# Optimization experiments

Measured on AMD Instinct MI355X. Metric: run time of the kernel, lower is better.

The kernel has to match this reference:

```python
import jax, jax.numpy as jnp
import numpy as np

ALPHA = 0.2  # leakyrelu negative slope and residual scale


def setup_inputs() -> dict:
    key = jax.random.key(0)
    k1, k2, k3, k4 = jax.random.split(key, 4)
    B, N, C, F = 8, 2048, 128, 128
    text = jax.random.normal(k1, (B, N, C), dtype=jnp.float32)
    adj = jax.random.uniform(k2, (B, N, N), dtype=jnp.float32)  # unused by the layer's math
    W = jax.random.normal(k3, (C, F), dtype=jnp.float32) * (1.0 / np.sqrt(C))
    a = jax.random.normal(k4, (2 * F, 1), dtype=jnp.float32) * 0.1
    return {"text": text, "adj": adj, "W": W, "a": a}


def reference(text, adj, W, a):
    # h: [B, N, F]
    h = jnp.matmul(text, W)
    Fdim = W.shape[1]
    a1 = a[:Fdim, 0]  # applies to source node i
    a2 = a[Fdim:, 0]  # applies to target node j
    e1 = jnp.einsum('bnf,f->bn', h, a1)  # [B, N]
    e2 = jnp.einsum('bnf,f->bn', h, a2)  # [B, N]
    # scores[b,i,j] = leakyrelu(a1.h_i + a2.h_j)  (same as concat-matmul in original)
    scores = jax.nn.leaky_relu(e1[:, :, None] + e2[:, None, :], negative_slope=ALPHA)
    attention = jax.nn.softmax(scores, axis=2)  # [B, N, N]; dropout off (eval)
    h_prime = jnp.matmul(attention, h)  # [B, N, F]
    return jax.nn.elu(h_prime + ALPHA * h)
```

## Files before the change

### kernel.cpp

```cpp
#include <hip/hip_runtime.h>
#include <hip/hip_bf16.h>

#define BB 8
#define NN 2048
#define CC 128
#define FF 128
#define ALPHA 0.2f
#define ROWS 16
#define WTPAD 136
#define CHN 256
#define CLEN 8
#define CSH 3

typedef __hip_bfloat16 bf16;
typedef __attribute__((ext_vector_type(8))) short short8;
typedef __attribute__((ext_vector_type(4))) float f32x4;
typedef unsigned long long u64;

__device__ __forceinline__ float ld1(const void* p, int i, int f32) {
    if (f32) return ((const float*)p)[i];
    return __bfloat162float(((const bf16*)p)[i]);
}
__device__ __forceinline__ float2 ld2(const void* p, int pair, int f32) {
    if (f32) return ((const float2*)p)[pair];
    __hip_bfloat162 v = ((const __hip_bfloat162*)p)[pair];
    return make_float2(__bfloat162float(v.x), __bfloat162float(v.y));
}
__device__ __forceinline__ u64 shfl_xor_u64(u64 v, int mask) {
    int lo = (int)(unsigned)(v & 0xFFFFFFFFull);
    int hi = (int)(unsigned)(v >> 32);
    lo = __shfl_xor(lo, mask, 64);
    hi = __shfl_xor(hi, mask, 64);
    return ((u64)(unsigned)hi << 32) | (unsigned)lo;
}

__global__ __launch_bounds__(256) void k_prep(const void* __restrict__ text,
                                              const void* __restrict__ W,
                                              const void* __restrict__ a,
                                              int* __restrict__ flag,
                                              float* __restrict__ wa1,
                                              float* __restrict__ wa2,
                                              ushort* __restrict__ WT) {
    __shared__ int cnt;
    __shared__ float aL[2 * FF];
    const int t = threadIdx.x;
    if (t == 0) cnt = 0;
    __syncthreads();
    const ushort2* p = (const ushort2*)text;
    int local = 0;
    for (int i = t; i < 1024; i += 256) {
        ushort2 v = p[i];
        float f = __uint_as_float(((unsigned)v.x) << 16);
        if (!(fabsf(f) <= 100.f)) local++;
    }
    atomicAdd(&cnt, local);
    __syncthreads();
    const int f32 = (cnt >= 64) ? 1 : 0;

    if (blockIdx.x == 0) {
        if (t == 0) flag[0] = f32;
        aL[t] = ld1(a, t, f32);
        __syncthreads();
        if (t < CC) {
            float s1 = 0.f, s2 = 0.f;
            for (int f = 0; f < FF; f += 4) {
                float w0 = ld1(W, t * FF + f, f32);
                float w1 = ld1(W, t * FF + f + 1, f32);
                float w2 = ld1(W, t * FF + f + 2, f32);
                float w3 = ld1(W, t * FF + f + 3, f32);
                s1 += w0 * aL[f] + w1 * aL[f + 1] + w2 * aL[f + 2] + w3 * aL[f + 3];
                s2 += w0 * aL[FF + f] + w1 * aL[FF + f + 1] + w2 * aL[FF + f + 2] + w3 * aL[FF + f + 3];
            }
            wa1[t] = s1; wa2[t] = s2;
        }
    } else {
        const int base = (blockIdx.x - 1) * 2048;
        for (int i = 0; i < 8; ++i) {
            int idx = base + i * 256 + t;
            int cc = idx >> 7, f = idx & 127;
            float v = ld1(W, idx, f32);
            bf16 b = __float2bfloat16(v);
            WT[f * CC + cc] = *(const ushort*)&b;
        }
    }
}

__global__ __launch_bounds__(256) void k_e(const void* __restrict__ text,
                                           const float* __restrict__ wa1,
                                           const float* __restrict__ wa2,
                                           float* __restrict__ e1,
                                           float* __restrict__ e2,
                                           const int* __restrict__ flag) {
    const int f32 = *flag;
    const int wave = threadIdx.x >> 6;
    const int lane = threadIdx.x & 63;
    const int row = blockIdx.x * 4 + wave;
    float2 tv = ld2(text, row * (CC / 2) + lane, f32);
    float s1 = tv.x * wa1[2 * lane] + tv.y * wa1[2 * lane + 1];
    float s2 = tv.x * wa2[2 * lane] + tv.y * wa2[2 * lane + 1];
#pragma unroll
    for (int off = 32; off > 0; off >>= 1) {
        s1 += __shfl_down(s1, off, 64);
        s2 += __shfl_down(s2, off, 64);
    }
    if (lane == 0) { e1[row] = s1; e2[row] = s2; }
}

__global__ __launch_bounds__(1024) void k_sort(const float* __restrict__ e2,
                                               const float* __restrict__ e1,
                                               float* __restrict__ e2s,
                                               int* __restrict__ sidx,
                                               float* __restrict__ rig) {
    __shared__ u64 lk[NN];
    __shared__ float es[NN];
    __shared__ float Z1L[NN + 1];
    __shared__ float Z2L[NN + 1];
    __shared__ float2 wtot[16];
    __shared__ float2 woff[16];
    const int b = blockIdx.x;
    const int t = threadIdx.x;

    float f0 = e2[b * NN + 2 * t], f1 = e2[b * NN + 2 * t + 1];
    unsigned m0 = __float_as_uint(f0); m0 = (m0 & 0x80000000u) ? ~m0 : (m0 | 0x80000000u);
    unsigned m1 = __float_as_uint(f1); m1 = (m1 & 0x80000000u) ? ~m1 : (m1 | 0x80000000u);
    u64 s0 = ((u64)m0 << 32) | (unsigned)(2 * t);
    u64 s1 = ((u64)m1 << 32) | (unsigned)(2 * t + 1);

    for (int size = 2; size <= NN; size <<= 1) {
        const bool up = (((2 * t) & size) == 0);
        for (int stride = size >> 1; stride >= 1; stride >>= 1) {
            if (stride == 1) {
                u64 mn = s0 < s1 ? s0 : s1;
                u64 mx = s0 < s1 ? s1 : s0;
                s0 = up ? mn : mx;
                s1 = up ? mx : mn;
            } else if (stride <= 64) {
                const int m = stride >> 1;
                u64 p0 = shfl_xor_u64(s0, m);
                u64 p1 = shfl_xor_u64(s1, m);
                const bool keepmin = (((t & m) == 0) == up);
                s0 = keepmin ? (s0 < p0 ? s0 : p0) : (s0 < p0 ? p0 : s0);
                s1 = keepmin ? (s1 < p1 ? s1 : p1) : (s1 < p1 ? p1 : s1);
            } else {
                lk[2 * t] = s0; lk[2 * t + 1] = s1;
                __syncthreads();
                u64 p0 = lk[(2 * t) ^ stride];
                u64 p1 = lk[(2 * t + 1) ^ stride];
                const bool keepmin = ((((2 * t) & stride) == 0) == up);
                s0 = keepmin ? (s0 < p0 ? s0 : p0) : (s0 < p0 ? p0 : s0);
                s1 = keepmin ? (s1 < p1 ? s1 : p1) : (s1 < p1 ? p1 : s1);
                __syncthreads();
            }
        }
    }

    unsigned k0 = (unsigned)(s0 >> 32), k1 = (unsigned)(s1 >> 32);
    float v0 = __uint_as_float((k0 & 0x80000000u) ? (k0 ^ 0x80000000u) : ~k0);
    float v1 = __uint_as_float((k1 & 0x80000000u) ? (k1 ^ 0x80000000u) : ~k1);
    es[2 * t] = v0;  es[2 * t + 1] = v1;
    e2s[b * NN + 2 * t] = v0;
    e2s[b * NN + 2 * t + 1] = v1;
    sidx[b * NN + 2 * t] = (int)(unsigned)(s0 & 0xFFFFFFFFull);
    sidx[b * NN + 2 * t + 1] = (int)(unsigned)(s1 & 0xFFFFFFFFull);

    float x0a = expf(v0), x0b = expf(ALPHA * v0);
    float x1a = expf(v1), x1b = expf(ALPHA * v1);
    float pa = x0a + x1a, pb = x0b + x1b;
    float sa = pa, sb = pb;
    const int lane = t & 63, wid = t >> 6;
#pragma unroll
    for (int off = 1; off < 64; off <<= 1) {
        float ya = __shfl_up(sa, off, 64);
        float yb = __shfl_up(sb, off, 64);
        if (lane >= off) { sa += ya; sb += yb; }
    }
    if (lane == 63) wtot[wid] = make_float2(sa, sb);
    __syncthreads();
    if (t == 0) {
        float ra = 0.f, rb = 0.f;
        for (int w2 = 0; w2 < 16; ++w2) {
            float2 tt = wtot[w2];
            woff[w2] = make_float2(ra, rb);
            ra += tt.x; rb += tt.y;
        }
    }
    __syncthreads();
    float2 o = woff[wid];
    float pre_a = o.x + sa - pa, pre_b = o.y + sb - pb;
    if (t == 0) { Z1L[0] = 0.f; Z2L[0] = 0.f; }
    Z1L[2 * t + 1] = pre_a + x0a;  Z2L[2 * t + 1] = pre_b + x0b;
    Z1L[2 * t + 2] = pre_a + pa;   Z2L[2 * t + 2] = pre_b + pb;
    __syncthreads();

    const float ZN = Z1L[NN];
#pragma unroll
    for (int rr = 0; rr < 2; ++rr) {
        const int r = t + rr * 1024;
        float ev = e1[b * NN + r];
        float w1 = expf(ev), w2 = expf(ALPHA * ev);
        float thr = -ev;
        int lo = 0, hi = NN;
        while (lo < hi) {
            int mid = (lo + hi) >> 1;
            if (es[mid] <= thr) lo = mid + 1; else hi = mid;
        }
        float den = w1 * (ZN - Z1L[lo]) + w2 * Z2L[lo];
        den = fmaxf(den, 1e-30f);
        ((float4*)rig)[b * NN + r] = make_float4(__int_as_float(lo), w1, w2, 1.f / den);
    }
}

__global__ __launch_bounds__(128) void k_tot(const void* __restrict__ text,
                                             const float* __restrict__ e2s,
                                             const int* __restrict__ sidx,
                                             float* __restrict__ T1,
                                             float* __restrict__ T2,
                                             const int* __restrict__ flag) {
    const int f32 = *flag;
    const int b = blockIdx.x / CHN, ch = blockIdx.x % CHN;
    const int c = threadIdx.x;
    float r1 = 0.f, r2 = 0.f;
    const int k0 = ch * CLEN;
#pragma unroll
    for (int kk = 0; kk < CLEN; ++kk) {
        int k = k0 + kk;
        float v = e2s[b * NN + k];
        int j = sidx[b * NN + k];
        float x = ld1(text, (b * NN + j) * CC + c, f32);
        r1 += expf(v) * x;
        r2 += expf(ALPHA * v) * x;
    }
    T1[(b * (CHN + 1) + ch) * CC + c] = r1;
    T2[(b * (CHN + 1) + ch) * CC + c] = r2;
}

__global__ __launch_bounds__(256) void k_scan2(float* __restrict__ T1,
                                               float* __restrict__ T2) {
    __shared__ float2 wt[4];
    const int b = blockIdx.x >> 7, c = blockIdx.x & 127;
    const int ch = threadIdx.x;
    float* P1 = T1 + (size_t)(b * (CHN + 1)) * CC + c;
    float* P2 = T2 + (size_t)(b * (CHN + 1)) * CC + c;
    const float t1 = P1[ch * CC];
    const float t2 = P2[ch * CC];
    float s1 = t1, s2 = t2;
    const int lane = ch & 63, wid = ch >> 6;
#pragma unroll
    for (int off = 1; off < 64; off <<= 1) {
        float y1 = __shfl_up(s1, off, 64);
        float y2 = __shfl_up(s2, off, 64);
        if (lane >= off) { s1 += y1; s2 += y2; }
    }
    if (lane == 63) wt[wid] = make_float2(s1, s2);
    __syncthreads();
    float o1 = 0.f, o2 = 0.f;
#pragma unroll
    for (int w2 = 0; w2 < 4; ++w2)
        if (w2 < wid) { o1 += wt[w2].x; o2 += wt[w2].y; }
    P1[ch * CC] = o1 + s1 - t1;
    P2[ch * CC] = o2 + s2 - t2;
    if (ch == CHN - 1) { P1[CHN * CC] = o1 + s1; P2[CHN * CC] = o2 + s2; }
}

__global__ __launch_bounds__(256) void k_out(const void* __restrict__ text,
                                             const ushort* __restrict__ WT,
                                             const float* __restrict__ T1,
                                             const float* __restrict__ T2,
                                             const float* __restrict__ e2s,
                                             const int* __restrict__ sidx,
                                             const float* __restrict__ rig,
                                             void* __restrict__ out,
                                             const int* __restrict__ flag) {
    __shared__ ushort WTl[FF * WTPAD];
    __shared__ ushort ul[ROWS * WTPAD];
    __shared__ float4 ri[ROWS];
    const int f32 = *flag;
    const int t = threadIdx.x;
    const int b = blockIdx.x / (NN / ROWS);
    const int r0 = (blockIdx.x % (NN / ROWS)) * ROWS;

    {
        const uint4* src = (const uint4*)WT;
#pragma unroll
        for (int i = 0; i < 8; ++i) {
            int idx = i * 256 + t;
            uint4 v = src[idx];
            int f = idx >> 4, cb = idx & 15;
            *(uint4*)&WTl[f * WTPAD + cb * 8] = v;
        }
    }
    if (t < ROWS) ri[t] = ((const float4*)rig)[b * NN + r0 + t];
    __syncthreads();

    {
        const int c = t & 127;
        const int g = t >> 7;
        const float* CB1 = T1 + (size_t)(b * (CHN + 1)) * CC + c;
        const float* CB2 = T2 + (size_t)(b * (CHN + 1)) * CC + c;
        const float* e2sb = e2s + b * NN;
        const int* sxb = sidx + b * NN;
        const float S1 = CB1[CHN * CC];
#pragma unroll
        for (int q = 0; q < 8; ++q) {
            const int rr = g * 8 + q;
            float4 info = ri[rr];
            const int k = __builtin_amdgcn_readfirstlane(__float_as_int(info.x));
            const int c0 = k >> CSH;
            float P1 = CB1[c0 * CC];
            float P2 = CB2[c0 * CC];
            const int j0 = c0 * CLEN;
            const int cnt = k - j0;
            if (cnt > 0) {
                float vv[CLEN - 1]; int jj[CLEN - 1];
#pragma unroll
                for (int i = 0; i < CLEN - 1; ++i) {
                    vv[i] = e2sb[j0 + i];
                    jj[i] = sxb[j0 + i];
                }
#pragma unroll
                for (int i = 0; i < CLEN - 1; ++i) {
                    if (i < cnt) {
                        float x = ld1(text, (b * NN + jj[i]) * CC + c, f32);
                        P1 += expf(vv[i]) * x;
                        P2 += expf(ALPHA * vv[i]) * x;
                    }
                }
            }
            float tc = ld1(text, (b * NN + r0 + rr) * CC + c, f32);
            float u = (info.y * (S1 - P1) + info.z * P2) * info.w + ALPHA * tc;
            bf16 ub = __float2bfloat16(u);
            ul[rr * WTPAD + c] = *(const ushort*)&ub;
        }
    }
    __syncthreads();

    {
        const int wv = t >> 6;
        const int lane = t & 63;
        const int m = lane & 15;
        const int quad = lane >> 4;
        f32x4 acc0 = {0.f, 0.f, 0.f, 0.f};
        f32x4 acc1 = {0.f, 0.f, 0.f, 0.f};
        const int f0 = (wv * 2 + 0) * 16 + m;
        const int f1 = (wv * 2 + 1) * 16 + m;
#pragma unroll
        for (int kt = 0; kt < 4; ++kt) {
            const int ko = kt * 32 + quad * 8;
            short8 afrag = *(const short8*)&ul[m * WTPAD + ko];
            short8 bf0 = *(const short8*)&WTl[f0 * WTPAD + ko];
            short8 bf1 = *(const short8*)&WTl[f1 * WTPAD + ko];
            acc0 = __builtin_amdgcn_mfma_f32_16x16x32_bf16(afrag, bf0, acc0, 0, 0, 0);
            acc1 = __builtin_amdgcn_mfma_f32_16x16x32_bf16(afrag, bf1, acc1, 0, 0, 0);
        }
#pragma unroll
        for (int ft = 0; ft < 2; ++ft) {
            f32x4 acc = ft ? acc1 : acc0;
            const int f = (wv * 2 + ft) * 16 + m;
#pragma unroll
            for (int reg = 0; reg < 4; ++reg) {
                const int urow = quad * 4 + reg;
                float x = acc[reg];
                float y = x > 0.f ? x : expm1f(x);
                const int orow = b * NN + r0 + urow;
                if (f32) ((float*)out)[orow * FF + f] = y;
                else     ((bf16*)out)[orow * FF + f] = __float2bfloat16(y);
            }
        }
    }
}

extern "C" void kernel_launch(void* const* d_in, const int* in_sizes, int n_in,
                              void* d_out, int out_size, void* d_ws, size_t ws_size,
                              hipStream_t stream) {
    const void* text = d_in[0];
    const void* Wp   = (n_in >= 4) ? d_in[2] : d_in[1];
    const void* ap   = (n_in >= 4) ? d_in[3] : d_in[2];
    for (int i = 0; i < n_in; ++i) {
        int s = in_sizes[i];
        if (s == BB * NN * CC)      text = d_in[i];
        else if (s == CC * FF)      Wp = d_in[i];
        else if (s == 2 * FF)       ap = d_in[i];
    }

    float* w = (float*)d_ws;
    size_t off = 0;
    int*    flagp  = (int*)(w + off);      off += 16;
    float*  wa1    = w + off;              off += 128;
    float*  wa2    = w + off;              off += 128;
    ushort* WT     = (ushort*)(w + off);   off += 8192;
    float*  e1     = w + off;              off += BB * NN;
    float*  e2     = w + off;              off += BB * NN;
    float*  e2s    = w + off;              off += BB * NN;
    int*    sidx   = (int*)(w + off);      off += BB * NN;
    float*  rig    = w + off;              off += (size_t)4 * BB * NN;
    float*  T1     = w + off;              off += (size_t)BB * (CHN + 1) * CC;
    float*  T2     = w + off;              off += (size_t)BB * (CHN + 1) * CC;

    k_prep<<<9, 256, 0, stream>>>(text, Wp, ap, flagp, wa1, wa2, WT);
    k_e<<<BB * NN / 4, 256, 0, stream>>>(text, wa1, wa2, e1, e2, flagp);
    k_sort<<<BB, 1024, 0, stream>>>(e2, e1, e2s, sidx, rig);
    k_tot<<<BB * CHN, 128, 0, stream>>>(text, e2s, sidx, T1, T2, flagp);
    k_scan2<<<BB * CC, 256, 0, stream>>>(T1, T2);
    k_out<<<BB * NN / ROWS, 256, 0, stream>>>(text, WT, T1, T2, e2s, sidx,
                                              rig, d_out, flagp);
}
```

Before: 248.2 us.

## Fuse chunk-total, scan and output kernels into one cooperative persistent kernel

Merges the three trailing kernels (per-chunk totals, prefix scan, output with MFMA projection) into a single cooperative kernel. Grid-wide syncs separate the phases, and grid-stride loops cover the work. It also loads the W tile into LDS once per block instead of once per 16-row tile. This targets kernel launch gaps and repeated WT loads, at the cost of grid.sync overhead and a smaller persistent grid. If the cooperative launch fails, it falls back to three phase-specific launches.

Result: slower. 438.9 us (+76.8%).

```diff
diff --git a/kernel.cpp b/kernel.cpp
--- a/kernel.cpp
+++ b/kernel.cpp
@@ -1,5 +1,8 @@
 #include <hip/hip_runtime.h>
 #include <hip/hip_bf16.h>
+#include <hip/hip_cooperative_groups.h>
+
+namespace cg = cooperative_groups;
 
 #define BB 8
 #define NN 2048
@@ -210,76 +213,25 @@
     }
 }
 
-__global__ __launch_bounds__(128) void k_tot(const void* __restrict__ text,
-                                             const float* __restrict__ e2s,
-                                             const int* __restrict__ sidx,
-                                             float* __restrict__ T1,
-                                             float* __restrict__ T2,
-                                             const int* __restrict__ flag) {
-    const int f32 = *flag;
-    const int b = blockIdx.x / CHN, ch = blockIdx.x % CHN;
-    const int c = threadIdx.x;
-    float r1 = 0.f, r2 = 0.f;
-    const int k0 = ch * CLEN;
-#pragma unroll
-    for (int kk = 0; kk < CLEN; ++kk) {
-        int k = k0 + kk;
-        float v = e2s[b * NN + k];
-        int j = sidx[b * NN + k];
-        float x = ld1(text, (b * NN + j) * CC + c, f32);
-        r1 += expf(v) * x;
-        r2 += expf(ALPHA * v) * x;
-    }
-    T1[(b * (CHN + 1) + ch) * CC + c] = r1;
-    T2[(b * (CHN + 1) + ch) * CC + c] = r2;
-}
-
-__global__ __launch_bounds__(256) void k_scan2(float* __restrict__ T1,
-                                               float* __restrict__ T2) {
-    __shared__ float2 wt[4];
-    const int b = blockIdx.x >> 7, c = blockIdx.x & 127;
-    const int ch = threadIdx.x;
-    float* P1 = T1 + (size_t)(b * (CHN + 1)) * CC + c;
-    float* P2 = T2 + (size_t)(b * (CHN + 1)) * CC + c;
-    const float t1 = P1[ch * CC];
-    const float t2 = P2[ch * CC];
-    float s1 = t1, s2 = t2;
-    const int lane = ch & 63, wid = ch >> 6;
-#pragma unroll
-    for (int off = 1; off < 64; off <<= 1) {
-        float y1 = __shfl_up(s1, off, 64);
-        float y2 = __shfl_up(s2, off, 64);
-        if (lane >= off) { s1 += y1; s2 += y2; }
-    }
-    if (lane == 63) wt[wid] = make_float2(s1, s2);
-    __syncthreads();
-    float o1 = 0.f, o2 = 0.f;
-#pragma unroll
-    for (int w2 = 0; w2 < 4; ++w2)
-        if (w2 < wid) { o1 += wt[w2].x; o2 += wt[w2].y; }
-    P1[ch * CC] = o1 + s1 - t1;
-    P2[ch * CC] = o2 + s2 - t2;
-    if (ch == CHN - 1) { P1[CHN * CC] = o1 + s1; P2[CHN * CC] = o2 + s2; }
-}
-
-__global__ __launch_bounds__(256) void k_out(const void* __restrict__ text,
-                                             const ushort* __restrict__ WT,
-                                             const float* __restrict__ T1,
-                                             const float* __restrict__ T2,
-                                             const float* __restrict__ e2s,
-                                             const int* __restrict__ sidx,
-                                             const float* __restrict__ rig,
-                                             void* __restrict__ out,
-                                             const int* __restrict__ flag) {
+__global__ __launch_bounds__(256, 4) void k_fused(const void* __restrict__ text,
+                                                  const ushort* __restrict__ WT,
+                                                  float* __restrict__ T1,
+                                                  float* __restrict__ T2,
+                                                  const float* __restrict__ e2s,
+                                                  const int* __restrict__ sidx,
+                                                  const float* __restrict__ rig,
+                                                  void* __restrict__ out,
+                                                  const int* __restrict__ flag,
+                                                  int plo, int phi) {
+    cg::grid_group grid = cg::this_grid();
     __shared__ ushort WTl[FF * WTPAD];
     __shared__ ushort ul[ROWS * WTPAD];
     __shared__ float4 ri[ROWS];
+    __shared__ float2 wt[4];
+    const int t = threadIdx.x;
     const int f32 = *flag;
-    const int t = threadIdx.x;
-    const int b = blockIdx.x / (NN / ROWS);
-    const int r0 = (blockIdx.x % (NN / ROWS)) * ROWS;
-
-    {
+
+    if (phi >= 2) {
         const uint4* src = (const uint4*)WT;
 #pragma unroll
         for (int i = 0; i < 8; ++i) {
@@ -289,82 +241,142 @@
             *(uint4*)&WTl[f * WTPAD + cb * 8] = v;
         }
     }
-    if (t < ROWS) ri[t] = ((const float4*)rig)[b * NN + r0 + t];
-    __syncthreads();
-
-    {
-        const int c = t & 127;
-        const int g = t >> 7;
-        const float* CB1 = T1 + (size_t)(b * (CHN + 1)) * CC + c;
-        const float* CB2 = T2 + (size_t)(b * (CHN + 1)) * CC + c;
-        const float* e2sb = e2s + b * NN;
-        const int* sxb = sidx + b * NN;
-        const float S1 = CB1[CHN * CC];
-#pragma unroll
-        for (int q = 0; q < 8; ++q) {
-            const int rr = g * 8 + q;
-            float4 info = ri[rr];
-            const int k = __builtin_amdgcn_readfirstlane(__float_as_int(info.x));
-            const int c0 = k >> CSH;
-            float P1 = CB1[c0 * CC];
-            float P2 = CB2[c0 * CC];
-            const int j0 = c0 * CLEN;
-            const int cnt = k - j0;
-            if (cnt > 0) {
-                float vv[CLEN - 1]; int jj[CLEN - 1];
-#pragma unroll
-                for (int i = 0; i < CLEN - 1; ++i) {
-                    vv[i] = e2sb[j0 + i];
-                    jj[i] = sxb[j0 + i];
+
+    if (plo <= 0 && 0 <= phi) {
+        for (int it = blockIdx.x; it < BB * CHN / 2; it += gridDim.x) {
+            const int gch = it * 2 + (t >> 7);
+            const int b = gch >> 8, ch = gch & (CHN - 1);
+            const int c = t & 127;
+            float r1 = 0.f, r2 = 0.f;
+            const int k0 = ch * CLEN;
+#pragma unroll
+            for (int kk = 0; kk < CLEN; ++kk) {
+                int k = k0 + kk;
+                float v = e2s[b * NN + k];
+                int j = sidx[b * NN + k];
+                float x = ld1(text, (b * NN + j) * CC + c, f32);
+                r1 += expf(v) * x;
+                r2 += expf(ALPHA * v) * x;
+            }
+            T1[(b * (CHN + 1) + ch) * CC + c] = r1;
+            T2[(b * (CHN + 1) + ch) * CC + c] = r2;
+        }
+    }
+    if (plo <= 0 && 1 <= phi) grid.sync();
+
+    if (plo <= 1 && 1 <= phi) {
+        for (int it = blockIdx.x; it < BB * CC; it += gridDim.x) {
+            const int b = it >> 7, c = it & 127;
+            const int ch = t;
+            float* P1 = T1 + (size_t)(b * (CHN + 1)) * CC + c;
+            float* P2 = T2 + (size_t)(b * (CHN + 1)) * CC + c;
+            const float t1 = P1[ch * CC];
+            const float t2 = P2[ch * CC];
+            float s1 = t1, s2 = t2;
+            const int lane = ch & 63, wid = ch >> 6;
+#pragma unroll
+            for (int off = 1; off < 64; off <<= 1) {
+                float y1 = __shfl_up(s1, off, 64);
+                float y2 = __shfl_up(s2, off, 64);
+                if (lane >= off) { s1 += y1; s2 += y2; }
+            }
+            if (lane == 63) wt[wid] = make_float2(s1, s2);
+            __syncthreads();
+            float o1 = 0.f, o2 = 0.f;
+#pragma unroll
+            for (int w2 = 0; w2 < 4; ++w2)
+                if (w2 < wid) { o1 += wt[w2].x; o2 += wt[w2].y; }
+            P1[ch * CC] = o1 + s1 - t1;
+            P2[ch * CC] = o2 + s2 - t2;
+            if (ch == CHN - 1) { P1[CHN * CC] = o1 + s1; P2[CHN * CC] = o2 + s2; }
+            __syncthreads();
+        }
+    }
+    if (plo <= 1 && 2 <= phi) grid.sync();
+
+    if (plo <= 2 && 2 <= phi) {
+        for (int it = blockIdx.x; it < BB * NN / ROWS; it += gridDim.x) {
+            const int b = it / (NN / ROWS);
+            const int r0 = (it % (NN / ROWS)) * ROWS;
+            if (t < ROWS) ri[t] = ((const float4*)rig)[b * NN + r0 + t];
+            __syncthreads();
+
+            {
+                const int c = t & 127;
+                const int g = t >> 7;
+                const float* CB1 = T1 + (size_t)(b * (CHN + 1)) * CC + c;
+                const float* CB2 = T2 + (size_t)(b * (CHN + 1)) * CC + c;
+                const float* e2sb = e2s + b * NN;
+                const int* sxb = sidx + b * NN;
+                const float S1 = CB1[CHN * CC];
+#pragma unroll
+                for (int q = 0; q < 8; ++q) {
+                    const int rr = g * 8 + q;
+                    float4 info = ri[rr];
+                    const int k = __builtin_amdgcn_readfirstlane(__float_as_int(info.x));
+                    const int c0 = k >> CSH;
+                    float P1 = CB1[c0 * CC];
+                    float P2 = CB2[c0 * CC];
+                    const int j0 = c0 * CLEN;
+                    const int cnt = k - j0;
+                    if (cnt > 0) {
+                        float vv[CLEN - 1]; int jj[CLEN - 1];
+#pragma unroll
+                        for (int i = 0; i < CLEN - 1; ++i) {
+                            vv[i] = e2sb[j0 + i];
+                            jj[i] = sxb[j0 + i];
+                        }
+#pragma unroll
+                        for (int i = 0; i < CLEN - 1; ++i) {
+                            if (i < cnt) {
+                                float x = ld1(text, (b * NN + jj[i]) * CC + c, f32);
+                                P1 += expf(vv[i]) * x;
+                                P2 += expf(ALPHA * vv[i]) * x;
+                            }
+                        }
+                    }
+                    float tc = ld1(text, (b * NN + r0 + rr) * CC + c, f32);
+                    float u = (info.y * (S1 - P1) + info.z * P2) * info.w + ALPHA * tc;
+                    bf16 ub = __float2bfloat16(u);
+                    ul[rr * WTPAD + c] = *(const ushort*)&ub;
                 }
-#pragma unroll
-                for (int i = 0; i < CLEN - 1; ++i) {
-                    if (i < cnt) {
-                        float x = ld1(text, (b * NN + jj[i]) * CC + c, f32);
-                        P1 += expf(vv[i]) * x;
-                        P2 += expf(ALPHA * vv[i]) * x;
+            }
+            __syncthreads();
+
+            {
+                const int wv = t >> 6;
+                const int lane = t & 63;
+                const int m = lane & 15;
+                const int quad = lane >> 4;
+                f32x4 acc0 = {0.f, 0.f, 0.f, 0.f};
+                f32x4 acc1 = {0.f, 0.f, 0.f, 0.f};
+                const int f0 = (wv * 2 + 0) * 16 + m;
+                const int f1 = (wv * 2 + 1) * 16 + m;
+#pragma unroll
+                for (int kt = 0; kt < 4; ++kt) {
+                    const int ko = kt * 32 + quad * 8;
+                    short8 afrag = *(const short8*)&ul[m * WTPAD + ko];
+                    short8 bf0 = *(const short8*)&WTl[f0 * WTPAD + ko];
+                    short8 bf1 = *(const short8*)&WTl[f1 * WTPAD + ko];
+                    acc0 = __builtin_amdgcn_mfma_f32_16x16x32_bf16(afrag, bf0, acc0, 0, 0, 0);
+                    acc1 = __builtin_amdgcn_mfma_f32_16x16x32_bf16(afrag, bf1, acc1, 0, 0, 0);
+                }
+#pragma unroll
+                for (int ft = 0; ft < 2; ++ft) {
+                    f32x4 acc = ft ? acc1 : acc0;
+                    const int f = (wv * 2 + ft) * 16 + m;
+#pragma unroll
+                    for (int reg = 0; reg < 4; ++reg) {
+                        const int urow = quad * 4 + reg;
+                        float x = acc[reg];
+                        float y = x > 0.f ? x : expm1f(x);
+                        const int orow = b * NN + r0 + urow;
+                        if (f32) ((float*)out)[orow * FF + f] = y;
+                        else     ((bf16*)out)[orow * FF + f] = __float2bfloat16(y);
                     }
                 }
             }
-            float tc = ld1(text, (b * NN + r0 + rr) * CC + c, f32);
-            float u = (info.y * (S1 - P1) + info.z * P2) * info.w + ALPHA * tc;
-            bf16 ub = __float2bfloat16(u);
-            ul[rr * WTPAD + c] = *(const ushort*)&ub;
-        }
-    }
-    __syncthreads();
-
-    {
-        const int wv = t >> 6;
-        const int lane = t & 63;
-        const int m = lane & 15;
-        const int quad = lane >> 4;
-        f32x4 acc0 = {0.f, 0.f, 0.f, 0.f};
-        f32x4 acc1 = {0.f, 0.f, 0.f, 0.f};
-        const int f0 = (wv * 2 + 0) * 16 + m;
-        const int f1 = (wv * 2 + 1) * 16 + m;
-#pragma unroll
-        for (int kt = 0; kt < 4; ++kt) {
-            const int ko = kt * 32 + quad * 8;
-            short8 afrag = *(const short8*)&ul[m * WTPAD + ko];
-            short8 bf0 = *(const short8*)&WTl[f0 * WTPAD + ko];
-            short8 bf1 = *(const short8*)&WTl[f1 * WTPAD + ko];
-            acc0 = __builtin_amdgcn_mfma_f32_16x16x32_bf16(afrag, bf0, acc0, 0, 0, 0);
-            acc1 = __builtin_amdgcn_mfma_f32_16x16x32_bf16(afrag, bf1, acc1, 0, 0, 0);
-        }
-#pragma unroll
-        for (int ft = 0; ft < 2; ++ft) {
-            f32x4 acc = ft ? acc1 : acc0;
-            const int f = (wv * 2 + ft) * 16 + m;
-#pragma unroll
-            for (int reg = 0; reg < 4; ++reg) {
-                const int urow = quad * 4 + reg;
-                float x = acc[reg];
-                float y = x > 0.f ? x : expm1f(x);
-                const int orow = b * NN + r0 + urow;
-                if (f32) ((float*)out)[orow * FF + f] = y;
-                else     ((bf16*)out)[orow * FF + f] = __float2bfloat16(y);
-            }
+            __syncthreads();
         }
     }
 }
@@ -399,8 +411,29 @@
     k_prep<<<9, 256, 0, stream>>>(text, Wp, ap, flagp, wa1, wa2, WT);
     k_e<<<BB * NN / 4, 256, 0, stream>>>(text, wa1, wa2, e1, e2, flagp);
     k_sort<<<BB, 1024, 0, stream>>>(e2, e1, e2s, sidx, rig);
-    k_tot<<<BB * CHN, 128, 0, stream>>>(text, e2s, sidx, T1, T2, flagp);
-    k_scan2<<<BB * CC, 256, 0, stream>>>(T1, T2);
-    k_out<<<BB * NN / ROWS, 256, 0, stream>>>(text, WT, T1, T2, e2s, sidx,
-                                              rig, d_out, flagp);
-}
+
+    static int coop_grid = 0;
+    if (coop_grid == 0) {
+        int nb = 0;
+        hipOccupancyMaxActiveBlocksPerMultiprocessor(&nb, k_fused, 256, 0);
+        if (nb < 1) nb = 1;
+        long g = (long)nb * 256;
+        coop_grid = (int)(g > 1024 ? 1024 : g);
+    }
+    int plo = 0, phi = 2;
+    void* ka[11];
+    ka[0] = (void*)&text;  ka[1] = (void*)&WT;   ka[2] = (void*)&T1;
+    ka[3] = (void*)&T2;    ka[4] = (void*)&e2s;  ka[5] = (void*)&sidx;
+    ka[6] = (void*)&rig;   ka[7] = (void*)&d_out; ka[8] = (void*)&flagp;
+    ka[9] = (void*)&plo;   ka[10] = (void*)&phi;
+    hipError_t err = hipLaunchCooperativeKernel(k_fused, dim3(coop_grid), dim3(256),
+                                                ka, 0u, stream);
+    if (err != hipSuccess) {
+        k_fused<<<1024, 256, 0, stream>>>(text, WT, T1, T2, e2s, sidx, rig,
+                                          d_out, flagp, 0, 0);
+        k_fused<<<1024, 256, 0, stream>>>(text, WT, T1, T2, e2s, sidx, rig,
+                                          d_out, flagp, 1, 1);
+        k_fused<<<1024, 256, 0, stream>>>(text, WT, T1, T2, e2s, sidx, rig,
+                                          d_out, flagp, 2, 2);
+    }
+}
```

## Fuse score projection into sort kernel and use packed 32-bit sort keys

Applied to the files above, without the earlier changes.

Removes the separate e1/e2 projection kernel and computes both projections inside the per-batch sort kernel, keeping them in shared memory instead of writing them to global memory and reading them back. The bitonic sort now uses 32-bit keys that pack the truncated float key with an 11-bit index, which halves the shuffle and LDS traffic compared with 64-bit keys. Sorted values are recovered by indexing the shared e2 array. The binary search now compares packed keys. The cost is that the projection pass, which reads all of text, runs on only 8 blocks, and the truncated mantissa makes the ordering approximate for nearly equal scores.

Measured after the change: 269.0 us. 1.08x slower.

```diff
diff --git a/kernel.cpp b/kernel.cpp
--- a/kernel.cpp
+++ b/kernel.cpp
@@ -15,23 +15,10 @@
 typedef __hip_bfloat16 bf16;
 typedef __attribute__((ext_vector_type(8))) short short8;
 typedef __attribute__((ext_vector_type(4))) float f32x4;
-typedef unsigned long long u64;
 
 __device__ __forceinline__ float ld1(const void* p, int i, int f32) {
     if (f32) return ((const float*)p)[i];
     return __bfloat162float(((const bf16*)p)[i]);
-}
-__device__ __forceinline__ float2 ld2(const void* p, int pair, int f32) {
-    if (f32) return ((const float2*)p)[pair];
-    __hip_bfloat162 v = ((const __hip_bfloat162*)p)[pair];
-    return make_float2(__bfloat162float(v.x), __bfloat162float(v.y));
-}
-__device__ __forceinline__ u64 shfl_xor_u64(u64 v, int mask) {
-    int lo = (int)(unsigned)(v & 0xFFFFFFFFull);
-    int hi = (int)(unsigned)(v >> 32);
-    lo = __shfl_xor(lo, mask, 64);
-    hi = __shfl_xor(hi, mask, 64);
-    return ((u64)(unsigned)hi << 32) | (unsigned)lo;
 }
 
 __global__ __launch_bounds__(256) void k_prep(const void* __restrict__ text,
@@ -85,67 +72,96 @@
     }
 }
 
-__global__ __launch_bounds__(256) void k_e(const void* __restrict__ text,
-                                           const float* __restrict__ wa1,
-                                           const float* __restrict__ wa2,
-                                           float* __restrict__ e1,
-                                           float* __restrict__ e2,
-                                           const int* __restrict__ flag) {
-    const int f32 = *flag;
-    const int wave = threadIdx.x >> 6;
-    const int lane = threadIdx.x & 63;
-    const int row = blockIdx.x * 4 + wave;
-    float2 tv = ld2(text, row * (CC / 2) + lane, f32);
-    float s1 = tv.x * wa1[2 * lane] + tv.y * wa1[2 * lane + 1];
-    float s2 = tv.x * wa2[2 * lane] + tv.y * wa2[2 * lane + 1];
-#pragma unroll
-    for (int off = 32; off > 0; off >>= 1) {
-        s1 += __shfl_down(s1, off, 64);
-        s2 += __shfl_down(s2, off, 64);
-    }
-    if (lane == 0) { e1[row] = s1; e2[row] = s2; }
-}
-
-__global__ __launch_bounds__(1024) void k_sort(const float* __restrict__ e2,
-                                               const float* __restrict__ e1,
-                                               float* __restrict__ e2s,
-                                               int* __restrict__ sidx,
-                                               float* __restrict__ rig) {
-    __shared__ u64 lk[NN];
-    __shared__ float es[NN];
+__global__ __launch_bounds__(1024) void k_sortE(const void* __restrict__ text,
+                                                const float* __restrict__ wa1,
+                                                const float* __restrict__ wa2,
+                                                float* __restrict__ e2s,
+                                                int* __restrict__ sidx,
+                                                float* __restrict__ rig,
+                                                const int* __restrict__ flag) {
+    __shared__ unsigned ks[NN];
+    __shared__ float e1L[NN];
+    __shared__ float e2L[NN];
     __shared__ float Z1L[NN + 1];
     __shared__ float Z2L[NN + 1];
+    __shared__ float wa1L[CC], wa2L[CC];
     __shared__ float2 wtot[16];
     __shared__ float2 woff[16];
     const int b = blockIdx.x;
     const int t = threadIdx.x;
-
-    float f0 = e2[b * NN + 2 * t], f1 = e2[b * NN + 2 * t + 1];
+    const int f32 = *flag;
+
+    if (t < CC) { wa1L[t] = wa1[t]; wa2L[t] = wa2[t]; }
+    __syncthreads();
+    {
+        const int l = t & 7;
+        const int rg = t >> 3;
+        const size_t esz = f32 ? 4 : 2;
+        for (int it = 0; it < 16; ++it) {
+            const int r = it * 128 + rg;
+            const char* rowp = (const char*)text + (size_t)(b * NN + r) * CC * esz;
+            float s1 = 0.f, s2 = 0.f;
+            if (f32) {
+                const float4* rp = (const float4*)rowp;
+#pragma unroll
+                for (int i = 0; i < 4; ++i) {
+                    float4 q = rp[l * 4 + i];
+                    const int c0 = l * 16 + i * 4;
+                    s1 += q.x * wa1L[c0] + q.y * wa1L[c0 + 1] + q.z * wa1L[c0 + 2] + q.w * wa1L[c0 + 3];
+                    s2 += q.x * wa2L[c0] + q.y * wa2L[c0 + 1] + q.z * wa2L[c0 + 2] + q.w * wa2L[c0 + 3];
+                }
+            } else {
+                const uint4* rp = (const uint4*)rowp;
+#pragma unroll
+                for (int i = 0; i < 2; ++i) {
+                    uint4 q = rp[l * 2 + i];
+                    const int c0 = l * 16 + i * 8;
+                    unsigned wd[4] = {q.x, q.y, q.z, q.w};
+#pragma unroll
+                    for (int u = 0; u < 4; ++u) {
+                        float lo = __uint_as_float((wd[u] & 0xFFFFu) << 16);
+                        float hi = __uint_as_float(wd[u] & 0xFFFF0000u);
+                        s1 += lo * wa1L[c0 + 2 * u] + hi * wa1L[c0 + 2 * u + 1];
+                        s2 += lo * wa2L[c0 + 2 * u] + hi * wa2L[c0 + 2 * u + 1];
+                    }
+                }
+            }
+#pragma unroll
+            for (int m = 4; m >= 1; m >>= 1) {
+                s1 += __shfl_xor(s1, m, 64);
+                s2 += __shfl_xor(s2, m, 64);
+            }
+            if (l == 0) { e1L[r] = s1; e2L[r] = s2; }
+        }
+    }
+    __syncthreads();
+
+    float f0 = e2L[2 * t], f1 = e2L[2 * t + 1];
     unsigned m0 = __float_as_uint(f0); m0 = (m0 & 0x80000000u) ? ~m0 : (m0 | 0x80000000u);
     unsigned m1 = __float_as_uint(f1); m1 = (m1 & 0x80000000u) ? ~m1 : (m1 | 0x80000000u);
-    u64 s0 = ((u64)m0 << 32) | (unsigned)(2 * t);
-    u64 s1 = ((u64)m1 << 32) | (unsigned)(2 * t + 1);
+    unsigned s0 = (m0 & 0xFFFFF800u) | (unsigned)(2 * t);
+    unsigned s1 = (m1 & 0xFFFFF800u) | (unsigned)(2 * t + 1);
 
     for (int size = 2; size <= NN; size <<= 1) {
         const bool up = (((2 * t) & size) == 0);
         for (int stride = size >> 1; stride >= 1; stride >>= 1) {
             if (stride == 1) {
-                u64 mn = s0 < s1 ? s0 : s1;
-                u64 mx = s0 < s1 ? s1 : s0;
+                unsigned mn = s0 < s1 ? s0 : s1;
+                unsigned mx = s0 < s1 ? s1 : s0;
                 s0 = up ? mn : mx;
                 s1 = up ? mx : mn;
             } else if (stride <= 64) {
                 const int m = stride >> 1;
-                u64 p0 = shfl_xor_u64(s0, m);
-                u64 p1 = shfl_xor_u64(s1, m);
+                unsigned p0 = (unsigned)__shfl_xor((int)s0, m, 64);
+                unsigned p1 = (unsigned)__shfl_xor((int)s1, m, 64);
                 const bool keepmin = (((t & m) == 0) == up);
                 s0 = keepmin ? (s0 < p0 ? s0 : p0) : (s0 < p0 ? p0 : s0);
                 s1 = keepmin ? (s1 < p1 ? s1 : p1) : (s1 < p1 ? p1 : s1);
             } else {
-                lk[2 * t] = s0; lk[2 * t + 1] = s1;
+                ks[2 * t] = s0; ks[2 * t + 1] = s1;
                 __syncthreads();
-                u64 p0 = lk[(2 * t) ^ stride];
-                u64 p1 = lk[(2 * t + 1) ^ stride];
+                unsigned p0 = ks[(2 * t) ^ stride];
+                unsigned p1 = ks[(2 * t + 1) ^ stride];
                 const bool keepmin = ((((2 * t) & stride) == 0) == up);
                 s0 = keepmin ? (s0 < p0 ? s0 : p0) : (s0 < p0 ? p0 : s0);
                 s1 = keepmin ? (s1 < p1 ? s1 : p1) : (s1 < p1 ? p1 : s1);
@@ -154,14 +170,13 @@
         }
     }
 
-    unsigned k0 = (unsigned)(s0 >> 32), k1 = (unsigned)(s1 >> 32);
-    float v0 = __uint_as_float((k0 & 0x80000000u) ? (k0 ^ 0x80000000u) : ~k0);
-    float v1 = __uint_as_float((k1 & 0x80000000u) ? (k1 ^ 0x80000000u) : ~k1);
-    es[2 * t] = v0;  es[2 * t + 1] = v1;
+    ks[2 * t] = s0; ks[2 * t + 1] = s1;
+    const int i0 = (int)(s0 & 0x7FFu), i1 = (int)(s1 & 0x7FFu);
+    float v0 = e2L[i0], v1 = e2L[i1];
     e2s[b * NN + 2 * t] = v0;
     e2s[b * NN + 2 * t + 1] = v1;
-    sidx[b * NN + 2 * t] = (int)(unsigned)(s0 & 0xFFFFFFFFull);
-    sidx[b * NN + 2 * t + 1] = (int)(unsigned)(s1 & 0xFFFFFFFFull);
+    sidx[b * NN + 2 * t] = i0;
+    sidx[b * NN + 2 * t + 1] = i1;
 
     float x0a = expf(v0), x0b = expf(ALPHA * v0);
     float x1a = expf(v1), x1b = expf(ALPHA * v1);
@@ -196,13 +211,15 @@
 #pragma unroll
     for (int rr = 0; rr < 2; ++rr) {
         const int r = t + rr * 1024;
-        float ev = e1[b * NN + r];
+        float ev = e1L[r];
         float w1 = expf(ev), w2 = expf(ALPHA * ev);
-        float thr = -ev;
+        unsigned mt = __float_as_uint(-ev);
+        mt = (mt & 0x80000000u) ? ~mt : (mt | 0x80000000u);
+        const unsigned tk = mt | 0x7FFu;
         int lo = 0, hi = NN;
         while (lo < hi) {
             int mid = (lo + hi) >> 1;
-            if (es[mid] <= thr) lo = mid + 1; else hi = mid;
+            if (ks[mid] <= tk) lo = mid + 1; else hi = mid;
         }
         float den = w1 * (ZN - Z1L[lo]) + w2 * Z2L[lo];
         den = fmaxf(den, 1e-30f);
@@ -388,8 +405,6 @@
     float*  wa1    = w + off;              off += 128;
     float*  wa2    = w + off;              off += 128;
     ushort* WT     = (ushort*)(w + off);   off += 8192;
-    float*  e1     = w + off;              off += BB * NN;
-    float*  e2     = w + off;              off += BB * NN;
     float*  e2s    = w + off;              off += BB * NN;
     int*    sidx   = (int*)(w + off);      off += BB * NN;
     float*  rig    = w + off;              off += (size_t)4 * BB * NN;
@@ -397,8 +412,7 @@
     float*  T2     = w + off;              off += (size_t)BB * (CHN + 1) * CC;
 
     k_prep<<<9, 256, 0, stream>>>(text, Wp, ap, flagp, wa1, wa2, WT);
-    k_e<<<BB * NN / 4, 256, 0, stream>>>(text, wa1, wa2, e1, e2, flagp);
-    k_sort<<<BB, 1024, 0, stream>>>(e2, e1, e2s, sidx, rig);
+    k_sortE<<<BB, 1024, 0, stream>>>(text, wa1, wa2, e2s, sidx, rig, flagp);
     k_tot<<<BB * CHN, 128, 0, stream>>>(text, e2s, sidx, T1, T2, flagp);
     k_scan2<<<BB * CC, 256, 0, stream>>>(T1, T2);
     k_out<<<BB * NN / ROWS, 256, 0, stream>>>(text, WT, T1, T2, e2s, sidx,
```

## Replace per-batch bitonic sort with parallel counting-rank sort across blocks

Applied to the files above, without the earlier changes.

Per-batch bitonic sort on 8 single blocks is replaced by a rank kernel. It loads packed 32-bit keys (truncated float bits plus index) into LDS and computes each element's rank and threshold count by brute-force comparison, spread over 256 blocks. The threshold binary search moves into the same counting pass. The prefix-sum stage becomes its own kernel. Truncating the key mantissa makes near-equal values tie-broken by index and the threshold split approximate, which trades O(N^2) comparisons and slight precision for much more parallelism.

Result: faster. 238.7 us (-3.8%).

```diff
diff --git a/kernel.cpp b/kernel.cpp
--- a/kernel.cpp
+++ b/kernel.cpp
@@ -15,7 +15,6 @@
 typedef __hip_bfloat16 bf16;
 typedef __attribute__((ext_vector_type(8))) short short8;
 typedef __attribute__((ext_vector_type(4))) float f32x4;
-typedef unsigned long long u64;
 
 __device__ __forceinline__ float ld1(const void* p, int i, int f32) {
     if (f32) return ((const float*)p)[i];
@@ -25,13 +24,6 @@
     if (f32) return ((const float2*)p)[pair];
     __hip_bfloat162 v = ((const __hip_bfloat162*)p)[pair];
     return make_float2(__bfloat162float(v.x), __bfloat162float(v.y));
-}
-__device__ __forceinline__ u64 shfl_xor_u64(u64 v, int mask) {
-    int lo = (int)(unsigned)(v & 0xFFFFFFFFull);
-    int hi = (int)(unsigned)(v >> 32);
-    lo = __shfl_xor(lo, mask, 64);
-    hi = __shfl_xor(hi, mask, 64);
-    return ((u64)(unsigned)hi << 32) | (unsigned)lo;
 }
 
 __global__ __launch_bounds__(256) void k_prep(const void* __restrict__ text,
@@ -90,6 +82,7 @@
                                            const float* __restrict__ wa2,
                                            float* __restrict__ e1,
                                            float* __restrict__ e2,
+                                           unsigned* __restrict__ ukey,
                                            const int* __restrict__ flag) {
     const int f32 = *flag;
     const int wave = threadIdx.x >> 6;
@@ -103,16 +96,61 @@
         s1 += __shfl_down(s1, off, 64);
         s2 += __shfl_down(s2, off, 64);
     }
-    if (lane == 0) { e1[row] = s1; e2[row] = s2; }
-}
-
-__global__ __launch_bounds__(1024) void k_sort(const float* __restrict__ e2,
-                                               const float* __restrict__ e1,
-                                               float* __restrict__ e2s,
-                                               int* __restrict__ sidx,
-                                               float* __restrict__ rig) {
-    __shared__ u64 lk[NN];
-    __shared__ float es[NN];
+    if (lane == 0) {
+        e1[row] = s1; e2[row] = s2;
+        unsigned m = __float_as_uint(s2);
+        m = (m & 0x80000000u) ? ~m : (m | 0x80000000u);
+        ukey[row] = (m & 0xFFFFF800u) | (unsigned)(row & (NN - 1));
+    }
+}
+
+__global__ __launch_bounds__(256) void k_rank(const unsigned* __restrict__ ukey,
+                                              const float* __restrict__ e1,
+                                              const float* __restrict__ e2,
+                                              float* __restrict__ e2s,
+                                              int* __restrict__ sidx,
+                                              int* __restrict__ lor) {
+    __shared__ unsigned kL[NN];
+    const int b = blockIdx.x >> 5;
+    const int seg = blockIdx.x & 31;
+    const int t = threadIdx.x;
+    {
+        const uint4* src = (const uint4*)(ukey + b * NN);
+        ((uint4*)kL)[t] = src[t];
+        ((uint4*)kL)[256 + t] = src[256 + t];
+    }
+    __syncthreads();
+    const int lane = t & 63;
+    const int wv = t >> 6;
+    const int rl = wv * 16 + (lane >> 2);
+    const int quarter = lane & 3;
+    const int r = seg * 64 + rl;
+    const unsigned my = kL[r];
+    const float ev = e1[b * NN + r];
+    unsigned mt = __float_as_uint(-ev);
+    mt = (mt & 0x80000000u) ? ~mt : (mt | 0x80000000u);
+    const unsigned tk = mt | 0x7FFu;
+    int rank = 0, lo = 0;
+    const uint4* q4 = (const uint4*)&kL[quarter * 512];
+#pragma unroll 4
+    for (int j = 0; j < 128; ++j) {
+        uint4 q = q4[j];
+        rank += (q.x < my) + (q.y < my) + (q.z < my) + (q.w < my);
+        lo   += (q.x <= tk) + (q.y <= tk) + (q.z <= tk) + (q.w <= tk);
+    }
+    rank += __shfl_xor(rank, 1, 64); lo += __shfl_xor(lo, 1, 64);
+    rank += __shfl_xor(rank, 2, 64); lo += __shfl_xor(lo, 2, 64);
+    if (quarter == 0) {
+        e2s[b * NN + rank] = e2[b * NN + r];
+        sidx[b * NN + rank] = r;
+        lor[b * NN + r] = lo;
+    }
+}
+
+__global__ __launch_bounds__(1024) void k_scanZ(const float* __restrict__ e2s,
+                                                const float* __restrict__ e1,
+                                                const int* __restrict__ lor,
+                                                float* __restrict__ rig) {
     __shared__ float Z1L[NN + 1];
     __shared__ float Z2L[NN + 1];
     __shared__ float2 wtot[16];
@@ -120,49 +158,8 @@
     const int b = blockIdx.x;
     const int t = threadIdx.x;
 
-    float f0 = e2[b * NN + 2 * t], f1 = e2[b * NN + 2 * t + 1];
-    unsigned m0 = __float_as_uint(f0); m0 = (m0 & 0x80000000u) ? ~m0 : (m0 | 0x80000000u);
-    unsigned m1 = __float_as_uint(f1); m1 = (m1 & 0x80000000u) ? ~m1 : (m1 | 0x80000000u);
-    u64 s0 = ((u64)m0 << 32) | (unsigned)(2 * t);
-    u64 s1 = ((u64)m1 << 32) | (unsigned)(2 * t + 1);
-
-    for (int size = 2; size <= NN; size <<= 1) {
-        const bool up = (((2 * t) & size) == 0);
-        for (int stride = size >> 1; stride >= 1; stride >>= 1) {
-            if (stride == 1) {
-                u64 mn = s0 < s1 ? s0 : s1;
-                u64 mx = s0 < s1 ? s1 : s0;
-                s0 = up ? mn : mx;
-                s1 = up ? mx : mn;
-            } else if (stride <= 64) {
-                const int m = stride >> 1;
-                u64 p0 = shfl_xor_u64(s0, m);
-                u64 p1 = shfl_xor_u64(s1, m);
-                const bool keepmin = (((t & m) == 0) == up);
-                s0 = keepmin ? (s0 < p0 ? s0 : p0) : (s0 < p0 ? p0 : s0);
-                s1 = keepmin ? (s1 < p1 ? s1 : p1) : (s1 < p1 ? p1 : s1);
-            } else {
-                lk[2 * t] = s0; lk[2 * t + 1] = s1;
-                __syncthreads();
-                u64 p0 = lk[(2 * t) ^ stride];
-                u64 p1 = lk[(2 * t + 1) ^ stride];
-                const bool keepmin = ((((2 * t) & stride) == 0) == up);
-                s0 = keepmin ? (s0 < p0 ? s0 : p0) : (s0 < p0 ? p0 : s0);
-                s1 = keepmin ? (s1 < p1 ? s1 : p1) : (s1 < p1 ? p1 : s1);
-                __syncthreads();
-            }
-        }
-    }
-
-    unsigned k0 = (unsigned)(s0 >> 32), k1 = (unsigned)(s1 >> 32);
-    float v0 = __uint_as_float((k0 & 0x80000000u) ? (k0 ^ 0x80000000u) : ~k0);
-    float v1 = __uint_as_float((k1 & 0x80000000u) ? (k1 ^ 0x80000000u) : ~k1);
-    es[2 * t] = v0;  es[2 * t + 1] = v1;
-    e2s[b * NN + 2 * t] = v0;
-    e2s[b * NN + 2 * t + 1] = v1;
-    sidx[b * NN + 2 * t] = (int)(unsigned)(s0 & 0xFFFFFFFFull);
-    sidx[b * NN + 2 * t + 1] = (int)(unsigned)(s1 & 0xFFFFFFFFull);
-
+    float2 vv = *(const float2*)&e2s[b * NN + 2 * t];
+    const float v0 = vv.x, v1 = vv.y;
     float x0a = expf(v0), x0b = expf(ALPHA * v0);
     float x1a = expf(v1), x1b = expf(ALPHA * v1);
     float pa = x0a + x1a, pb = x0b + x1b;
@@ -198,12 +195,7 @@
         const int r = t + rr * 1024;
         float ev = e1[b * NN + r];
         float w1 = expf(ev), w2 = expf(ALPHA * ev);
-        float thr = -ev;
-        int lo = 0, hi = NN;
-        while (lo < hi) {
-            int mid = (lo + hi) >> 1;
-            if (es[mid] <= thr) lo = mid + 1; else hi = mid;
-        }
+        const int lo = lor[b * NN + r];
         float den = w1 * (ZN - Z1L[lo]) + w2 * Z2L[lo];
         den = fmaxf(den, 1e-30f);
         ((float4*)rig)[b * NN + r] = make_float4(__int_as_float(lo), w1, w2, 1.f / den);
@@ -384,21 +376,24 @@
 
     float* w = (float*)d_ws;
     size_t off = 0;
-    int*    flagp  = (int*)(w + off);      off += 16;
-    float*  wa1    = w + off;              off += 128;
-    float*  wa2    = w + off;              off += 128;
-    ushort* WT     = (ushort*)(w + off);   off += 8192;
-    float*  e1     = w + off;              off += BB * NN;
-    float*  e2     = w + off;              off += BB * NN;
-    float*  e2s    = w + off;              off += BB * NN;
-    int*    sidx   = (int*)(w + off);      off += BB * NN;
-    float*  rig    = w + off;              off += (size_t)4 * BB * NN;
-    float*  T1     = w + off;              off += (size_t)BB * (CHN + 1) * CC;
-    float*  T2     = w + off;              off += (size_t)BB * (CHN + 1) * CC;
+    int*      flagp = (int*)(w + off);      off += 16;
+    float*    wa1   = w + off;              off += 128;
+    float*    wa2   = w + off;              off += 128;
+    ushort*   WT    = (ushort*)(w + off);   off += 8192;
+    float*    e1    = w + off;              off += BB * NN;
+    float*    e2    = w + off;              off += BB * NN;
+    unsigned* ukey  = (unsigned*)(w + off); off += BB * NN;
+    float*    e2s   = w + off;              off += BB * NN;
+    int*      sidx  = (int*)(w + off);      off += BB * NN;
+    int*      lor   = (int*)(w + off);      off += BB * NN;
+    float*    rig   = w + off;              off += (size_t)4 * BB * NN;
+    float*    T1    = w + off;              off += (size_t)BB * (CHN + 1) * CC;
+    float*    T2    = w + off;              off += (size_t)BB * (CHN + 1) * CC;
 
     k_prep<<<9, 256, 0, stream>>>(text, Wp, ap, flagp, wa1, wa2, WT);
-    k_e<<<BB * NN / 4, 256, 0, stream>>>(text, wa1, wa2, e1, e2, flagp);
-    k_sort<<<BB, 1024, 0, stream>>>(e2, e1, e2s, sidx, rig);
+    k_e<<<BB * NN / 4, 256, 0, stream>>>(text, wa1, wa2, e1, e2, ukey, flagp);
+    k_rank<<<BB * 32, 256, 0, stream>>>(ukey, e1, e2, e2s, sidx, lor);
+    k_scanZ<<<BB, 1024, 0, stream>>>(e2s, e1, lor, rig);
     k_tot<<<BB * CHN, 128, 0, stream>>>(text, e2s, sidx, T1, T2, flagp);
     k_scan2<<<BB * CC, 256, 0, stream>>>(T1, T2);
     k_out<<<BB * NN / ROWS, 256, 0, stream>>>(text, WT, T1, T2, e2s, sidx,
```
